# Kernel tuning notes

Hardware: AMD Instinct MI355X
Metric: run time of the kernel (lower is better)

## Reference

```python
import jax, jax.numpy as jnp
import numpy as np

N_NODES = 50000
N_EDGES = 1600000
IN_FEATS = 128
ENC_H = 20
DEC_H = 64


def setup_inputs() -> dict:
    key = jax.random.key(0)
    ks = jax.random.split(key, 14)
    inp = {}
    inp["x"] = jax.random.normal(ks[0], (N_NODES, IN_FEATS), dtype=jnp.float32)
    inp["edge_index"] = jax.random.randint(ks[1], (2, N_EDGES), 0, N_NODES, dtype=jnp.int64)
    inp["node_id"] = 0
    inp["noise_normal"] = jax.random.normal(ks[2], (N_EDGES, ENC_H), dtype=jnp.float32)
    inp["noise_u"] = jax.random.uniform(ks[3], (N_EDGES, 1), dtype=jnp.float32)
    # parameters (glorot-ish init)
    def lin(k, fan_in, fan_out):
        s = 1.0 / np.sqrt(fan_in)
        return jax.random.uniform(k, (fan_in, fan_out), jnp.float32, -s, s)
    inp["W_gc"] = lin(ks[4], IN_FEATS, ENC_H)
    inp["b_gc"] = jnp.zeros((ENC_H,), jnp.float32)
    inp["W_mu"] = lin(ks[5], 3 * ENC_H, ENC_H)
    inp["b_mu"] = jnp.zeros((ENC_H,), jnp.float32)
    inp["W_var"] = lin(ks[6], 3 * ENC_H, ENC_H)
    inp["b_var"] = jnp.zeros((ENC_H,), jnp.float32)
    inp["W_d1"] = lin(ks[7], ENC_H, DEC_H)
    inp["b_d1"] = jnp.zeros((DEC_H,), jnp.float32)
    inp["W_d2"] = lin(ks[8], DEC_H, 1)
    inp["b_d2"] = jnp.zeros((1,), jnp.float32)
    return inp


def _gcn_conv(x, edge_index, W, b):
    """PyG-style GCNConv: add self-loops, symmetric D^-1/2 (A+I) D^-1/2 norm."""
    n = x.shape[0]
    sl = jnp.arange(n, dtype=edge_index.dtype)
    row = jnp.concatenate([edge_index[0], sl])  # source
    col = jnp.concatenate([edge_index[1], sl])  # target
    xw = x @ W  # [N, H]
    deg = jax.ops.segment_sum(jnp.ones_like(col, dtype=xw.dtype), col, num_segments=n)
    dinv = jnp.where(deg > 0, jax.lax.rsqrt(deg), 0.0)
    norm = dinv[row] * dinv[col]  # [E+N]
    out = jax.ops.segment_sum(xw[row] * norm[:, None], col, num_segments=n)
    return out + b


def reference(x, edge_index, node_id, noise_normal, noise_u,
              W_gc, b_gc, W_mu, b_mu, W_var, b_var, W_d1, b_d1, W_d2, b_d2):
    # GCN encoder
    x1 = jax.nn.relu(_gcn_conv(x, edge_index, W_gc, b_gc))  # [N, H]
    # per-edge concat: [src_embed | dst_embed | node_id_embed]
    rows, cols = edge_index[0], edge_index[1]
    node_embed = jnp.broadcast_to(x1[node_id][None, :], (rows.shape[0], x1.shape[1]))
    x2 = jnp.concatenate([x1[rows], x1[cols], node_embed], axis=1)  # [E, 3H]
    # variational heads + reparameterization
    mu = x2 @ W_mu + b_mu
    sigma = jnp.exp(x2 @ W_var + b_var)
    z = mu + sigma * noise_normal  # [E, H]
    # decoder MLP
    h = jax.nn.relu(z @ W_d1 + b_d1)
    sampling_weights = jax.nn.relu(h @ W_d2 + b_d2)  # [E, 1]
    # gumbel-sigmoid sample (training=True, bias=0.0 -> bias'=1e-4, temperature=1.0)
    bias = 0.0001
    eps = (bias - (1.0 - bias)) * noise_u + (1.0 - bias)
    gate = jnp.log(eps) - jnp.log(1.0 - eps) + sampling_weights
    return jax.nn.sigmoid(gate)
```

## Files before the change

### kernel.cpp

```cpp
#include <hip/hip_runtime.h>

#define NFEAT 128
#define H 20
#define DH 64
#define SCAN_T 1024
#define BE 64
#define NB 128
#define HW 12800

typedef __attribute__((ext_vector_type(8))) short short8;
typedef __attribute__((ext_vector_type(4))) float f32x4;

__device__ __forceinline__ unsigned short f2bf(float f) {
    union { float f; unsigned u; } v; v.f = f;
    unsigned r = v.u + 0x7fff + ((v.u >> 16) & 1);
    return (unsigned short)(r >> 16);
}
__device__ __forceinline__ unsigned pk2(unsigned short a, unsigned short b) {
    return (unsigned)a | ((unsigned)b << 16);
}

template <int CTRL>
__device__ __forceinline__ float dpp_add(float x) {
    int y = __builtin_amdgcn_update_dpp(0, __float_as_int(x), CTRL, 0xF, 0xF, true);
    return x + __int_as_float(y);
}
__device__ __forceinline__ float sum16(float x) {
    x = dpp_add<0xB1>(x);
    x = dpp_add<0x4E>(x);
    x = dpp_add<0x124>(x);
    x = dpp_add<0x128>(x);
    return x;
}

__global__ __launch_bounds__(256) void k_prep(const float* __restrict__ Wmu, const float* __restrict__ Wvar,
                                              const float* __restrict__ Wd1,
                                              const float* __restrict__ bmu, const float* __restrict__ bvar,
                                              unsigned short* __restrict__ Bh, unsigned short* __restrict__ Bd1,
                                              float* __restrict__ bcat, int* __restrict__ deg, int N) {
    int t = blockIdx.x * blockDim.x + threadIdx.x;
    if (t < N) deg[t] = 0;
    if (t < 512) {
        int f = t >> 6, l = t & 63;
        int tile = f >> 1, s = f & 1;
        int col = (tile & 1) * 16 + (l & 15);
        const float* W = (tile < 2) ? Wmu : Wvar;
#pragma unroll
        for (int j = 0; j < 8; j++) {
            int k = s * 32 + (l >> 4) * 8 + j;
            float v = (k < 3 * H && col < H) ? W[k * H + col] : 0.f;
            Bh[(size_t)f * 512 + l * 8 + j] = f2bf(v);
        }
    } else if (t < 768) {
        int f = (t - 512) >> 6, l = t & 63;
        int n = f * 16 + (l & 15);
#pragma unroll
        for (int j = 0; j < 8; j++) {
            int k = (l >> 4) * 8 + j;
            float v = (k < H) ? Wd1[k * DH + n] : 0.f;
            Bd1[(size_t)f * 512 + l * 8 + j] = f2bf(v);
        }
    } else if (t < 808) {
        int c = t - 768;
        bcat[c] = (c < H) ? bmu[c] : bvar[c - H];
    }
}


__global__ __launch_bounds__(512) void k_hist(const int* __restrict__ cols,
                                              unsigned* __restrict__ hist, int E, int N) {
    __shared__ unsigned h[HW];
    int wstride = (N + 3) >> 2;
    for (int i = threadIdx.x; i < wstride; i += 512) h[i] = 0;
    __syncthreads();
    int chunk = (E + NB - 1) / NB;
    int beg = blockIdx.x * chunk, end = min(beg + chunk, E);
    for (int i = beg + threadIdx.x; i < end; i += 512) {
        int c = __builtin_nontemporal_load(cols + i);
        atomicAdd(&h[c >> 2], 1u << ((c & 3) * 8));
    }
    __syncthreads();
    unsigned* dst = hist + (size_t)blockIdx.x * wstride;
    for (int i = threadIdx.x; i < wstride; i += 512) dst[i] = h[i];
}

__global__ __launch_bounds__(256) void k_sumbins(const unsigned* __restrict__ hist,
                                                 int* __restrict__ deg, int* __restrict__ chunkSum, int N) {
    __shared__ int sc[256];
    int c = blockIdx.x * 256 + threadIdx.x;
    int wstride = (N + 3) >> 2;
    int sh = (c & 3) * 8;
    int d = 0;
    if (c < N) {
#pragma unroll 4
        for (int b = 0; b < NB; b++) d += (hist[(size_t)b * wstride + (c >> 2)] >> sh) & 0xFF;
        deg[c] = d;
    }
    sc[threadIdx.x] = d;
    __syncthreads();
    for (int off = 128; off > 0; off >>= 1) {
        if (threadIdx.x < off) sc[threadIdx.x] += sc[threadIdx.x + off];
        __syncthreads();
    }
    if (threadIdx.x == 0) chunkSum[blockIdx.x] = sc[0];
}

__global__ __launch_bounds__(256) void k_scansmall(const int* __restrict__ chunkSum,
                                                   int* __restrict__ chunkOff, int nb) {
    __shared__ int sc[256];
    int t = threadIdx.x;
    int v0 = (t < nb) ? chunkSum[t] : 0;
    sc[t] = v0;
    __syncthreads();
    for (int off = 1; off < 256; off <<= 1) {
        int v = (t >= off) ? sc[t - off] : 0;
        __syncthreads();
        sc[t] += v;
        __syncthreads();
    }
    if (t < nb) chunkOff[t] = sc[t] - v0;
}

__global__ __launch_bounds__(256) void k_bases(const unsigned* __restrict__ hist,
                                               const int* __restrict__ chunkOff,
                                               unsigned char* __restrict__ delta,
                                               int* __restrict__ offsets, int N, int E) {
    __shared__ int sc[256];
    int c = blockIdx.x * 256 + threadIdx.x;
    int wstride = (N + 3) >> 2;
    int sh = (c & 3) * 8;
    int d = 0;
    if (c < N) {
#pragma unroll 4
        for (int b = 0; b < NB; b++) d += (hist[(size_t)b * wstride + (c >> 2)] >> sh) & 0xFF;
    }
    sc[threadIdx.x] = d;
    __syncthreads();
    for (int off = 1; off < 256; off <<= 1) {
        int v = (threadIdx.x >= off) ? sc[threadIdx.x - off] : 0;
        __syncthreads();
        sc[threadIdx.x] += v;
        __syncthreads();
    }
    if (c < N) {
        int base = chunkOff[blockIdx.x] + sc[threadIdx.x] - d;
        offsets[c] = base;
        int run = 0;
#pragma unroll 4
        for (int b = 0; b < NB; b++) {
            delta[(size_t)b * N + c] = (unsigned char)run;
            run += (hist[(size_t)b * wstride + (c >> 2)] >> sh) & 0xFF;
        }
    }
    if (blockIdx.x == 0 && threadIdx.x == 0) offsets[N] = E;
}

__global__ __launch_bounds__(512) void k_place(const int* __restrict__ rows, const int* __restrict__ cols,
                                               const int* __restrict__ offsets,
                                               const unsigned char* __restrict__ delta,
                                               unsigned short* __restrict__ srcs, int E, int N) {
    __shared__ unsigned h[HW];
    int wstride = (N + 3) >> 2;
    for (int i = threadIdx.x; i < wstride; i += 512) h[i] = 0;
    __syncthreads();
    int chunk = (E + NB - 1) / NB;
    int beg = blockIdx.x * chunk, end = min(beg + chunk, E);
    const unsigned char* mydelta = delta + (size_t)blockIdx.x * N;
    for (int i = beg + threadIdx.x; i < end; i += 512) {
        int c = __builtin_nontemporal_load(cols + i);
        int r = __builtin_nontemporal_load(rows + i);
        int sh = (c & 3) * 8;
        unsigned old = atomicAdd(&h[c >> 2], 1u << sh);
        int rank = (old >> sh) & 0xFF;
        int pos = offsets[c] + (int)mydelta[c] + rank;
        srcs[pos] = (unsigned short)r;
    }
}

__global__ __launch_bounds__(256) void k_deg(const int* __restrict__ cols, int* __restrict__ deg, int E) {
    int t = blockIdx.x * blockDim.x + threadIdx.x;
    if (t < E) atomicAdd(&deg[cols[t]], 1);
}

__global__ __launch_bounds__(SCAN_T) void k_scan(const int* __restrict__ deg, int* __restrict__ offsets,
                                                 int* __restrict__ cursor, int N) {
    __shared__ int sums[SCAN_T];
    int t = threadIdx.x;
    int chunk = (N + SCAN_T - 1) / SCAN_T;
    int beg = t * chunk;
    int end = min(beg + chunk, N);
    int s = 0;
    for (int i = beg; i < end; i++) s += deg[i];
    sums[t] = s;
    __syncthreads();
    for (int off = 1; off < SCAN_T; off <<= 1) {
        int v = (t >= off) ? sums[t - off] : 0;
        __syncthreads();
        sums[t] += v;
        __syncthreads();
    }
    int run = (t == 0) ? 0 : sums[t - 1];
    for (int i = beg; i < end; i++) {
        offsets[i] = run;
        cursor[i] = run;
        run += deg[i];
    }
    if (t == SCAN_T - 1) offsets[N] = sums[SCAN_T - 1];
}

__global__ __launch_bounds__(256) void k_bucket_csr(const int* __restrict__ rows, const int* __restrict__ cols,
                                                    int* __restrict__ cursor, int* __restrict__ srcs, int E) {
    int e = blockIdx.x * blockDim.x + threadIdx.x;
    if (e >= E) return;
    int pos = atomicAdd(&cursor[cols[e]], 1);
    srcs[pos] = rows[e];
}

__global__ __launch_bounds__(256) void k_xw_xs(const float* __restrict__ x, const float* __restrict__ Wgc,
                                               const int* __restrict__ deg,
                                               float* __restrict__ xs, int N) {
    __shared__ float Ws[NFEAT * H];
    for (int i = threadIdx.x; i < NFEAT * H; i += blockDim.x) Ws[i] = Wgc[i];
    __syncthreads();
    int n = blockIdx.x * blockDim.x + threadIdx.x;
    if (n >= N) return;
    float acc[H];
#pragma unroll
    for (int j = 0; j < H; j++) acc[j] = 0.f;
    const float4* x4 = (const float4*)(x + (size_t)n * NFEAT);
#pragma unroll 4
    for (int k4 = 0; k4 < NFEAT / 4; k4++) {
        float4 xv = x4[k4];
#pragma unroll
        for (int s = 0; s < 4; s++) {
            float xk = (s == 0) ? xv.x : (s == 1) ? xv.y : (s == 2) ? xv.z : xv.w;
            const float4* wrow = (const float4*)(Ws + (k4 * 4 + s) * H);
#pragma unroll
            for (int q = 0; q < 5; q++) {
                float4 w = wrow[q];
                acc[q * 4 + 0] += xk * w.x;
                acc[q * 4 + 1] += xk * w.y;
                acc[q * 4 + 2] += xk * w.z;
                acc[q * 4 + 3] += xk * w.w;
            }
        }
    }
    float di = rsqrtf((float)(deg[n] + 1));
    float4* o = (float4*)(xs + (size_t)n * H);
#pragma unroll
    for (int q = 0; q < 5; q++)
        o[q] = make_float4(acc[q * 4 + 0] * di, acc[q * 4 + 1] * di, acc[q * 4 + 2] * di, acc[q * 4 + 3] * di);
}

template <typename IT>
__device__ __forceinline__ void gather_core16(const float* __restrict__ xs, const IT* __restrict__ idx,
                                              int beg, int end, int n, int sl, int degn,
                                              const float* __restrict__ bgc, unsigned short* __restrict__ x1b) {
    float acc[H];
    if (sl == 0) {
        const float4* self = (const float4*)(xs + (size_t)n * H);
#pragma unroll
        for (int q = 0; q < 5; q++) {
            float4 v = self[q];
            acc[q * 4 + 0] = v.x; acc[q * 4 + 1] = v.y; acc[q * 4 + 2] = v.z; acc[q * 4 + 3] = v.w;
        }
    } else {
#pragma unroll
        for (int j = 0; j < H; j++) acc[j] = 0.f;
    }
#pragma unroll 2
    for (int i = beg + sl; i < end; i += 16) {
        int r = (int)__builtin_nontemporal_load(idx + i);
        const float4* p = (const float4*)(xs + (size_t)r * H);
#pragma unroll
        for (int q = 0; q < 5; q++) {
            float4 v = p[q];
            acc[q * 4 + 0] += v.x; acc[q * 4 + 1] += v.y; acc[q * 4 + 2] += v.z; acc[q * 4 + 3] += v.w;
        }
    }
#pragma unroll
    for (int j = 0; j < H; j++) acc[j] = sum16(acc[j]);
    if (sl == 0) {
        float di = rsqrtf((float)(degn + 1));
        unsigned o[10];
#pragma unroll
        for (int j = 0; j < 10; j++) {
            float v0 = fmaxf(di * acc[2 * j] + bgc[2 * j], 0.f);
            float v1 = fmaxf(di * acc[2 * j + 1] + bgc[2 * j + 1], 0.f);
            o[j] = pk2(f2bf(v0), f2bf(v1));
        }
        unsigned* dst = (unsigned*)(x1b + (size_t)n * H);
        *(uint4*)dst = make_uint4(o[0], o[1], o[2], o[3]);
        *(uint4*)(dst + 4) = make_uint4(o[4], o[5], o[6], o[7]);
        *(uint2*)(dst + 8) = make_uint2(o[8], o[9]);
    }
}

__global__ __launch_bounds__(256) void k_gather_csr16(const float* __restrict__ xs, const unsigned short* __restrict__ srcs,
                                                      const int* __restrict__ offsets, const int* __restrict__ deg,
                                                      const float* __restrict__ bgc,
                                                      unsigned short* __restrict__ x1b, int N) {
    int wave = (blockIdx.x * 256 + threadIdx.x) >> 6;
    int lane = threadIdx.x & 63;
    int n = wave * 4 + (lane >> 4);
    if (n >= N) return;
    gather_core16(xs, srcs, offsets[n], offsets[n + 1], n, lane & 15, deg[n], bgc, x1b);
}

__global__ __launch_bounds__(256) void k_gather_csr(const float* __restrict__ xs, const int* __restrict__ srcs,
                                                    const int* __restrict__ offsets, const int* __restrict__ deg,
                                                    const float* __restrict__ bgc,
                                                    unsigned short* __restrict__ x1b, int N) {
    int wave = (blockIdx.x * 256 + threadIdx.x) >> 6;
    int lane = threadIdx.x & 63;
    int n = wave * 4 + (lane >> 4);
    if (n >= N) return;
    gather_core16(xs, srcs, offsets[n], offsets[n + 1], n, lane & 15, deg[n], bgc, x1b);
}

__global__ __launch_bounds__(256, 8) void k_mlp(
    const unsigned short* __restrict__ x1b, const int* __restrict__ rows, const int* __restrict__ cols,
    const int* __restrict__ node_id, const float* __restrict__ noise_n, const float* __restrict__ noise_u,
    const unsigned short* __restrict__ Bh, const unsigned short* __restrict__ Bd1g,
    const float* __restrict__ bcat, const float* __restrict__ b_d1,
    const float* __restrict__ W_d2, const float* __restrict__ b_d2,
    float* __restrict__ out, int E) {

    __shared__ __align__(16) unsigned short x2s[BE * 72];
    __shared__ __align__(16) unsigned short A2[BE * 44];

    int tid = threadIdx.x;
    int e0 = blockIdx.x * BE;
    int l = tid & 63, w = tid >> 6;
    int m = l & 15, quad = l >> 4;
    int erow0 = w * 16 + quad * 4;

    float nz0[4], nz1[4];
#pragma unroll
    for (int r4 = 0; r4 < 4; r4++) {
        int e = e0 + erow0 + r4;
        int ec = (e < E) ? e : 0;
        nz0[r4] = noise_n[(size_t)ec * H + m];
        nz1[r4] = (m < 4) ? noise_n[(size_t)ec * H + 16 + m] : 0.f;
    }

    {
        int le = tid >> 2, p = tid & 3;
        int e = e0 + le; if (e >= E) e = E - 1;
        int r = rows[e], c = cols[e];
        int nid = node_id[0];
#pragma unroll
        for (int ii = 0; ii < 4; ii++) {
            int i = p + ii * 4;
            unsigned* dst = (unsigned*)((char*)x2s + le * 144 + i * 8);
            if (i < 15) {
                int node = (i < 5) ? r : (i < 10) ? c : nid;
                int cc = (i < 5) ? i : (i < 10) ? i - 5 : i - 10;
                uint2 v = *(const uint2*)((const char*)x1b + (size_t)node * 40 + cc * 8);
                dst[0] = v.x;
                dst[1] = v.y;
            } else {
                dst[0] = 0u; dst[1] = 0u;
            }
        }
    }
    __syncthreads();

    f32x4 accs[4];
    {
        const char* arow = (const char*)x2s + (w * 16 + m) * 144 + quad * 16;
        short8 a0 = *(const short8*)(arow);
        short8 a1 = *(const short8*)(arow + 64);
#pragma unroll
        for (int t4 = 0; t4 < 4; t4++) {
            f32x4 acc = {0.f, 0.f, 0.f, 0.f};
            short8 b0 = *(const short8*)(Bh + (t4 * 2 + 0) * 512 + l * 8);
            short8 b1 = *(const short8*)(Bh + (t4 * 2 + 1) * 512 + l * 8);
            acc = __builtin_amdgcn_mfma_f32_16x16x32_bf16(a0, b0, acc, 0, 0, 0);
            acc = __builtin_amdgcn_mfma_f32_16x16x32_bf16(a1, b1, acc, 0, 0, 0);
            accs[t4] = acc;
        }
    }

    {
        float bm0 = bcat[m];
        float bv0 = bcat[20 + m];
        float bm1 = (m < 4) ? bcat[16 + m] : 0.f;
        float bv1 = (m < 4) ? bcat[36 + m] : 0.f;
#pragma unroll
        for (int r4 = 0; r4 < 4; r4++) {
            float z0 = accs[0][r4] + bm0 + expf(accs[2][r4] + bv0) * nz0[r4];
            *(unsigned short*)((char*)A2 + (erow0 + r4) * 88 + m * 2) = f2bf(z0);
            unsigned short z1v = 0;
            if (m < 4) z1v = f2bf(accs[1][r4] + bm1 + expf(accs[3][r4] + bv1) * nz1[r4]);
            *(unsigned short*)((char*)A2 + (erow0 + r4) * 88 + (16 + m) * 2) = z1v;
        }
    }
    __syncthreads();

    {
        short8 a2 = *(const short8*)((const char*)A2 + (w * 16 + m) * 88 + quad * 16);
        float p0 = 0.f, p1 = 0.f, p2 = 0.f, p3 = 0.f;
#pragma unroll
        for (int t4 = 0; t4 < 4; t4++) {
            f32x4 acc = {0.f, 0.f, 0.f, 0.f};
            short8 bb = *(const short8*)(Bd1g + t4 * 512 + l * 8);
            acc = __builtin_amdgcn_mfma_f32_16x16x32_bf16(a2, bb, acc, 0, 0, 0);
            int col = t4 * 16 + m;
            float bias = b_d1[col], wo = W_d2[col];
            p0 += fmaxf(acc[0] + bias, 0.f) * wo;
            p1 += fmaxf(acc[1] + bias, 0.f) * wo;
            p2 += fmaxf(acc[2] + bias, 0.f) * wo;
            p3 += fmaxf(acc[3] + bias, 0.f) * wo;
        }
        p0 = sum16(p0); p1 = sum16(p1); p2 = sum16(p2); p3 = sum16(p3);
        if (m < 4) {
            float swv = (m == 0) ? p0 : (m == 1) ? p1 : (m == 2) ? p2 : p3;
            int leo = w * 16 + quad * 4 + m;
            int e = e0 + leo;
            if (e < E) {
                float sw = fmaxf(swv + b_d2[0], 0.f);
                float u = noise_u[e];
                float ev = 0.9999f - 0.9998f * u;
                float t = expf(-sw);
                out[e] = ev / (ev + (1.f - ev) * t);
            }
        }
    }
}

extern "C" void kernel_launch(void* const* d_in, const int* in_sizes, int n_in,
                              void* d_out, int out_size, void* d_ws, size_t ws_size,
                              hipStream_t stream) {
    const int N = in_sizes[0] / NFEAT;
    const int E = in_sizes[1] / 2;

    const float* x       = (const float*)d_in[0];
    const int*   ei      = (const int*)d_in[1];
    const int*   rows    = ei;
    const int*   cols    = ei + E;
    const int*   node_id = (const int*)d_in[2];
    const float* noise_n = (const float*)d_in[3];
    const float* noise_u = (const float*)d_in[4];
    const float* Wgc  = (const float*)d_in[5];
    const float* bgc  = (const float*)d_in[6];
    const float* Wmu  = (const float*)d_in[7];
    const float* bmu  = (const float*)d_in[8];
    const float* Wvar = (const float*)d_in[9];
    const float* bvar = (const float*)d_in[10];
    const float* Wd1  = (const float*)d_in[11];
    const float* bd1  = (const float*)d_in[12];
    const float* Wd2  = (const float*)d_in[13];
    const float* bd2  = (const float*)d_in[14];
    float* out = (float*)d_out;

    const int B = 256;
    int gN  = (N + B - 1) / B;
    int gG  = (N + 15) / 16;
    int gE  = (E + B - 1) / B;
    int gM  = (E + BE - 1) / BE;
    int nBins = (N + 255) / 256;

    char* ws = (char*)d_ws;
    size_t o_deg     = 0;
    size_t o_off     = o_deg  + (((size_t)N * 4 + 255) & ~255ULL);
    size_t o_csum    = o_off  + (((size_t)(N + 1) * 4 + 255) & ~255ULL);
    size_t o_coff    = o_csum + 1024;
    size_t o_hist    = o_coff + 1024;
    size_t wstride   = (size_t)((N + 3) >> 2);
    size_t o_delta   = o_hist  + ((NB * wstride * 4 + 255) & ~255ULL);
    size_t o_srcs    = o_delta + (((size_t)NB * N + 255) & ~255ULL);
    size_t o_xs      = o_srcs  + (((size_t)E * 2 + 255) & ~255ULL);
    size_t o_x1b     = o_xs    + (((size_t)N * H * 4 + 255) & ~255ULL);
    size_t o_Bh      = o_x1b   + (((size_t)N * H * 2 + 255) & ~255ULL);
    size_t o_Bd1     = o_Bh    + 8192;
    size_t o_bcat    = o_Bd1   + 4096;
    size_t need      = o_bcat  + 256;

    bool main_path = (ws_size >= need) && (N <= 4 * HW) && (N < 65536) && (nBins <= 256);

    if (main_path) {
        int*   deg     = (int*)(ws + o_deg);
        int*   offsets = (int*)(ws + o_off);
        int*   csum    = (int*)(ws + o_csum);
        int*   coff    = (int*)(ws + o_coff);
        unsigned* hist = (unsigned*)(ws + o_hist);
        unsigned char* delta = (unsigned char*)(ws + o_delta);
        unsigned short* srcs = (unsigned short*)(ws + o_srcs);
        float* xs      = (float*)(ws + o_xs);
        unsigned short* x1b  = (unsigned short*)(ws + o_x1b);
        unsigned short* Bh   = (unsigned short*)(ws + o_Bh);
        unsigned short* Bd1  = (unsigned short*)(ws + o_Bd1);
        float* bcat    = (float*)(ws + o_bcat);

        k_prep<<<gN, B, 0, stream>>>(Wmu, Wvar, Wd1, bmu, bvar, Bh, Bd1, bcat, deg, N);
        k_hist<<<NB, 512, 0, stream>>>(cols, hist, E, N);
        k_sumbins<<<nBins, B, 0, stream>>>(hist, deg, csum, N);
        k_scansmall<<<1, B, 0, stream>>>(csum, coff, nBins);
        k_bases<<<nBins, B, 0, stream>>>(hist, coff, delta, offsets, N, E);
        k_xw_xs<<<gN, B, 0, stream>>>(x, Wgc, deg, xs, N);
        k_place<<<NB, 512, 0, stream>>>(rows, cols, offsets, delta, srcs, E, N);
        k_gather_csr16<<<gG, B, 0, stream>>>(xs, srcs, offsets, deg, bgc, x1b, N);
        k_mlp<<<gM, B, 0, stream>>>(x1b, rows, cols, node_id, noise_n, noise_u,
                                    Bh, Bd1, bcat, bd1, Wd2, bd2, out, E);
    } else {
        int*   deg     = (int*)ws;
        int*   offsets = (int*)(ws + 200000);
        int*   cursor  = (int*)(ws + 400016);
        int*   srcs    = (int*)(ws + 600016);
        float* xs      = (float*)(ws + 7000016);
        unsigned short* x1b = (unsigned short*)(ws + 11000016);
        unsigned short* Bh  = (unsigned short*)(ws + 13000016);
        unsigned short* Bd1 = (unsigned short*)(ws + 13008208);
        float* bcat    = (float*)(ws + 13012304);

        k_prep<<<gN, B, 0, stream>>>(Wmu, Wvar, Wd1, bmu, bvar, Bh, Bd1, bcat, deg, N);
        k_deg<<<gE, B, 0, stream>>>(cols, deg, E);
        k_scan<<<1, SCAN_T, 0, stream>>>(deg, offsets, cursor, N);
        k_bucket_csr<<<gE, B, 0, stream>>>(rows, cols, cursor, srcs, E);
        k_xw_xs<<<gN, B, 0, stream>>>(x, Wgc, deg, xs, N);
        k_gather_csr<<<gG, B, 0, stream>>>(xs, srcs, offsets, deg, bgc, x1b, N);
        k_mlp<<<gM, B, 0, stream>>>(x1b, rows, cols, node_id, noise_n, noise_u,
                                    Bh, Bd1, bcat, bd1, Wd2, bd2, out, E);
    }
}
```

Measured before the change: 448.2 us.

## Fold node_id embedding into head bias, fuse degree sums into histogram pass

The node_id third of the concatenated edge feature is the same for every edge, so its product with W_mu/W_var is computed once by the thread handling node_id in the gather kernel and folded into a per-call bias. The per-edge MLP then drops that gather and the K dimension shrinks to 40. The k_sumbins pass is removed: chunk sums are accumulated atomically in k_hist, and k_bases keeps per-bin counts in registers to write deg and the delta table without re-reading hist. NB grows to 192 and expf becomes __expf, which trades a little accuracy and adds register pressure in k_bases.

```diff
diff --git a/kernel.cpp b/kernel.cpp
--- a/kernel.cpp
+++ b/kernel.cpp
@@ -5,7 +5,7 @@
 #define DH 64
 #define SCAN_T 1024
 #define BE 64
-#define NB 128
+#define NB 192
 #define HW 12800
 
 typedef __attribute__((ext_vector_type(8))) short short8;
@@ -35,11 +35,11 @@
 
 __global__ __launch_bounds__(256) void k_prep(const float* __restrict__ Wmu, const float* __restrict__ Wvar,
                                               const float* __restrict__ Wd1,
-                                              const float* __restrict__ bmu, const float* __restrict__ bvar,
                                               unsigned short* __restrict__ Bh, unsigned short* __restrict__ Bd1,
-                                              float* __restrict__ bcat, int* __restrict__ deg, int N) {
+                                              int* __restrict__ deg, int* __restrict__ csum, int N) {
     int t = blockIdx.x * blockDim.x + threadIdx.x;
     if (t < N) deg[t] = 0;
+    if (t < 256) csum[t] = 0;
     if (t < 512) {
         int f = t >> 6, l = t & 63;
         int tile = f >> 1, s = f & 1;
@@ -48,7 +48,7 @@
 #pragma unroll
         for (int j = 0; j < 8; j++) {
             int k = s * 32 + (l >> 4) * 8 + j;
-            float v = (k < 3 * H && col < H) ? W[k * H + col] : 0.f;
+            float v = (k < 2 * H && col < H) ? W[k * H + col] : 0.f;
             Bh[(size_t)f * 512 + l * 8 + j] = f2bf(v);
         }
     } else if (t < 768) {
@@ -60,18 +60,18 @@
             float v = (k < H) ? Wd1[k * DH + n] : 0.f;
             Bd1[(size_t)f * 512 + l * 8 + j] = f2bf(v);
         }
-    } else if (t < 808) {
-        int c = t - 768;
-        bcat[c] = (c < H) ? bmu[c] : bvar[c - H];
-    }
-}
-
+    }
+}
 
 __global__ __launch_bounds__(512) void k_hist(const int* __restrict__ cols,
-                                              unsigned* __restrict__ hist, int E, int N) {
+                                              unsigned* __restrict__ hist, int* __restrict__ csum,
+                                              int E, int N) {
     __shared__ unsigned h[HW];
+    __shared__ int cs[256];
     int wstride = (N + 3) >> 2;
+    int nchunks = (N + 255) >> 8;
     for (int i = threadIdx.x; i < wstride; i += 512) h[i] = 0;
+    if (threadIdx.x < 256) cs[threadIdx.x] = 0;
     __syncthreads();
     int chunk = (E + NB - 1) / NB;
     int beg = blockIdx.x * chunk, end = min(beg + chunk, E);
@@ -81,28 +81,17 @@
     }
     __syncthreads();
     unsigned* dst = hist + (size_t)blockIdx.x * wstride;
-    for (int i = threadIdx.x; i < wstride; i += 512) dst[i] = h[i];
-}
-
-__global__ __launch_bounds__(256) void k_sumbins(const unsigned* __restrict__ hist,
-                                                 int* __restrict__ deg, int* __restrict__ chunkSum, int N) {
-    __shared__ int sc[256];
-    int c = blockIdx.x * 256 + threadIdx.x;
-    int wstride = (N + 3) >> 2;
-    int sh = (c & 3) * 8;
-    int d = 0;
-    if (c < N) {
-#pragma unroll 4
-        for (int b = 0; b < NB; b++) d += (hist[(size_t)b * wstride + (c >> 2)] >> sh) & 0xFF;
-        deg[c] = d;
-    }
-    sc[threadIdx.x] = d;
-    __syncthreads();
-    for (int off = 128; off > 0; off >>= 1) {
-        if (threadIdx.x < off) sc[threadIdx.x] += sc[threadIdx.x + off];
-        __syncthreads();
-    }
-    if (threadIdx.x == 0) chunkSum[blockIdx.x] = sc[0];
+    for (int i = threadIdx.x; i < wstride; i += 512) {
+        unsigned w = h[i];
+        dst[i] = w;
+        if (w) {
+            int s = (w & 0xFF) + ((w >> 8) & 0xFF) + ((w >> 16) & 0xFF) + (w >> 24);
+            atomicAdd(&cs[i >> 6], s);
+        }
+    }
+    __syncthreads();
+    for (int j = threadIdx.x; j < nchunks; j += 512)
+        if (cs[j]) atomicAdd(&csum[j], cs[j]);
 }
 
 __global__ __launch_bounds__(256) void k_scansmall(const int* __restrict__ chunkSum,
@@ -124,16 +113,25 @@
 __global__ __launch_bounds__(256) void k_bases(const unsigned* __restrict__ hist,
                                                const int* __restrict__ chunkOff,
                                                unsigned char* __restrict__ delta,
-                                               int* __restrict__ offsets, int N, int E) {
+                                               int* __restrict__ offsets, int* __restrict__ deg,
+                                               int N, int E) {
     __shared__ int sc[256];
     int c = blockIdx.x * 256 + threadIdx.x;
     int wstride = (N + 3) >> 2;
     int sh = (c & 3) * 8;
+    bool valid = c < N;
+    int cw = valid ? (c >> 2) : 0;
+    unsigned cnt[NB / 4];
     int d = 0;
-    if (c < N) {
-#pragma unroll 4
-        for (int b = 0; b < NB; b++) d += (hist[(size_t)b * wstride + (c >> 2)] >> sh) & 0xFF;
-    }
+#pragma unroll
+    for (int b = 0; b < NB; b++) {
+        unsigned w = hist[(size_t)b * wstride + cw];
+        unsigned byte = (w >> sh) & 0xFF;
+        if ((b & 3) == 0) cnt[b >> 2] = byte;
+        else cnt[b >> 2] |= byte << ((b & 3) * 8);
+        d += (int)byte;
+    }
+    if (!valid) d = 0;
     sc[threadIdx.x] = d;
     __syncthreads();
     for (int off = 1; off < 256; off <<= 1) {
@@ -142,14 +140,15 @@
         sc[threadIdx.x] += v;
         __syncthreads();
     }
-    if (c < N) {
+    if (valid) {
         int base = chunkOff[blockIdx.x] + sc[threadIdx.x] - d;
         offsets[c] = base;
+        deg[c] = d;
         int run = 0;
-#pragma unroll 4
+#pragma unroll
         for (int b = 0; b < NB; b++) {
             delta[(size_t)b * N + c] = (unsigned char)run;
-            run += (hist[(size_t)b * wstride + (c >> 2)] >> sh) & 0xFF;
+            run += (int)((cnt[b >> 2] >> ((b & 3) * 8)) & 0xFF);
         }
     }
     if (blockIdx.x == 0 && threadIdx.x == 0) offsets[N] = E;
@@ -255,7 +254,10 @@
 template <typename IT>
 __device__ __forceinline__ void gather_core16(const float* __restrict__ xs, const IT* __restrict__ idx,
                                               int beg, int end, int n, int sl, int degn,
-                                              const float* __restrict__ bgc, unsigned short* __restrict__ x1b) {
+                                              const float* __restrict__ bgc, unsigned short* __restrict__ x1b,
+                                              int nid, const float* __restrict__ Wmu, const float* __restrict__ Wvar,
+                                              const float* __restrict__ bmu, const float* __restrict__ bvar,
+                                              float* __restrict__ bcat2) {
     float acc[H];
     if (sl == 0) {
         const float4* self = (const float4*)(xs + (size_t)n * H);
@@ -280,49 +282,73 @@
     }
 #pragma unroll
     for (int j = 0; j < H; j++) acc[j] = sum16(acc[j]);
+    float di = rsqrtf((float)(degn + 1));
+    float x1f[H];
+#pragma unroll
+    for (int j = 0; j < H; j++) x1f[j] = fmaxf(di * acc[j] + bgc[j], 0.f);
     if (sl == 0) {
-        float di = rsqrtf((float)(degn + 1));
         unsigned o[10];
 #pragma unroll
-        for (int j = 0; j < 10; j++) {
-            float v0 = fmaxf(di * acc[2 * j] + bgc[2 * j], 0.f);
-            float v1 = fmaxf(di * acc[2 * j + 1] + bgc[2 * j + 1], 0.f);
-            o[j] = pk2(f2bf(v0), f2bf(v1));
-        }
+        for (int j = 0; j < 10; j++) o[j] = pk2(f2bf(x1f[2 * j]), f2bf(x1f[2 * j + 1]));
         unsigned* dst = (unsigned*)(x1b + (size_t)n * H);
         *(uint4*)dst = make_uint4(o[0], o[1], o[2], o[3]);
         *(uint4*)(dst + 4) = make_uint4(o[4], o[5], o[6], o[7]);
         *(uint2*)(dst + 8) = make_uint2(o[8], o[9]);
     }
+    if (n == nid) {
+#pragma unroll
+        for (int base = 0; base < 48; base += 16) {
+            int jj = base + sl;
+            if (jj < 40) {
+                bool ismu = jj < 20;
+                int col = ismu ? jj : jj - 20;
+                const float* W = ismu ? Wmu : Wvar;
+                float s = ismu ? bmu[col] : bvar[col];
+#pragma unroll
+                for (int k = 0; k < H; k++) s += x1f[k] * W[(2 * H + k) * H + col];
+                bcat2[jj] = s;
+            }
+        }
+    }
 }
 
 __global__ __launch_bounds__(256) void k_gather_csr16(const float* __restrict__ xs, const unsigned short* __restrict__ srcs,
                                                       const int* __restrict__ offsets, const int* __restrict__ deg,
                                                       const float* __restrict__ bgc,
-                                                      unsigned short* __restrict__ x1b, int N) {
+                                                      unsigned short* __restrict__ x1b,
+                                                      const int* __restrict__ node_id,
+                                                      const float* __restrict__ Wmu, const float* __restrict__ Wvar,
+                                                      const float* __restrict__ bmu, const float* __restrict__ bvar,
+                                                      float* __restrict__ bcat2, int N) {
     int wave = (blockIdx.x * 256 + threadIdx.x) >> 6;
     int lane = threadIdx.x & 63;
     int n = wave * 4 + (lane >> 4);
     if (n >= N) return;
-    gather_core16(xs, srcs, offsets[n], offsets[n + 1], n, lane & 15, deg[n], bgc, x1b);
+    gather_core16(xs, srcs, offsets[n], offsets[n + 1], n, lane & 15, deg[n], bgc, x1b,
+                  node_id[0], Wmu, Wvar, bmu, bvar, bcat2);
 }
 
 __global__ __launch_bounds__(256) void k_gather_csr(const float* __restrict__ xs, const int* __restrict__ srcs,
                                                     const int* __restrict__ offsets, const int* __restrict__ deg,
                                                     const float* __restrict__ bgc,
-                                                    unsigned short* __restrict__ x1b, int N) {
+                                                    unsigned short* __restrict__ x1b,
+                                                    const int* __restrict__ node_id,
+                                                    const float* __restrict__ Wmu, const float* __restrict__ Wvar,
+                                                    const float* __restrict__ bmu, const float* __restrict__ bvar,
+                                                    float* __restrict__ bcat2, int N) {
     int wave = (blockIdx.x * 256 + threadIdx.x) >> 6;
     int lane = threadIdx.x & 63;
     int n = wave * 4 + (lane >> 4);
     if (n >= N) return;
-    gather_core16(xs, srcs, offsets[n], offsets[n + 1], n, lane & 15, deg[n], bgc, x1b);
+    gather_core16(xs, srcs, offsets[n], offsets[n + 1], n, lane & 15, deg[n], bgc, x1b,
+                  node_id[0], Wmu, Wvar, bmu, bvar, bcat2);
 }
 
 __global__ __launch_bounds__(256, 8) void k_mlp(
     const unsigned short* __restrict__ x1b, const int* __restrict__ rows, const int* __restrict__ cols,
-    const int* __restrict__ node_id, const float* __restrict__ noise_n, const float* __restrict__ noise_u,
+    const float* __restrict__ noise_n, const float* __restrict__ noise_u,
     const unsigned short* __restrict__ Bh, const unsigned short* __restrict__ Bd1g,
-    const float* __restrict__ bcat, const float* __restrict__ b_d1,
+    const float* __restrict__ bcat2, const float* __restrict__ b_d1,
     const float* __restrict__ W_d2, const float* __restrict__ b_d2,
     float* __restrict__ out, int E) {
 
@@ -348,14 +374,13 @@
         int le = tid >> 2, p = tid & 3;
         int e = e0 + le; if (e >= E) e = E - 1;
         int r = rows[e], c = cols[e];
-        int nid = node_id[0];
 #pragma unroll
         for (int ii = 0; ii < 4; ii++) {
             int i = p + ii * 4;
             unsigned* dst = (unsigned*)((char*)x2s + le * 144 + i * 8);
-            if (i < 15) {
-                int node = (i < 5) ? r : (i < 10) ? c : nid;
-                int cc = (i < 5) ? i : (i < 10) ? i - 5 : i - 10;
+            if (i < 10) {
+                int node = (i < 5) ? r : c;
+                int cc = (i < 5) ? i : i - 5;
                 uint2 v = *(const uint2*)((const char*)x1b + (size_t)node * 40 + cc * 8);
                 dst[0] = v.x;
                 dst[1] = v.y;
@@ -383,16 +408,16 @@
     }
 
     {
-        float bm0 = bcat[m];
-        float bv0 = bcat[20 + m];
-        float bm1 = (m < 4) ? bcat[16 + m] : 0.f;
-        float bv1 = (m < 4) ? bcat[36 + m] : 0.f;
+        float bm0 = bcat2[m];
+        float bv0 = bcat2[20 + m];
+        float bm1 = (m < 4) ? bcat2[16 + m] : 0.f;
+        float bv1 = (m < 4) ? bcat2[36 + m] : 0.f;
 #pragma unroll
         for (int r4 = 0; r4 < 4; r4++) {
-            float z0 = accs[0][r4] + bm0 + expf(accs[2][r4] + bv0) * nz0[r4];
+            float z0 = accs[0][r4] + bm0 + __expf(accs[2][r4] + bv0) * nz0[r4];
             *(unsigned short*)((char*)A2 + (erow0 + r4) * 88 + m * 2) = f2bf(z0);
             unsigned short z1v = 0;
-            if (m < 4) z1v = f2bf(accs[1][r4] + bm1 + expf(accs[3][r4] + bv1) * nz1[r4]);
+            if (m < 4) z1v = f2bf(accs[1][r4] + bm1 + __expf(accs[3][r4] + bv1) * nz1[r4]);
             *(unsigned short*)((char*)A2 + (erow0 + r4) * 88 + (16 + m) * 2) = z1v;
         }
     }
@@ -422,7 +447,7 @@
                 float sw = fmaxf(swv + b_d2[0], 0.f);
                 float u = noise_u[e];
                 float ev = 0.9999f - 0.9998f * u;
-                float t = expf(-sw);
+                float t = __expf(-sw);
                 out[e] = ev / (ev + (1.f - ev) * t);
             }
         }
@@ -474,8 +499,8 @@
     size_t o_x1b     = o_xs    + (((size_t)N * H * 4 + 255) & ~255ULL);
     size_t o_Bh      = o_x1b   + (((size_t)N * H * 2 + 255) & ~255ULL);
     size_t o_Bd1     = o_Bh    + 8192;
-    size_t o_bcat    = o_Bd1   + 4096;
-    size_t need      = o_bcat  + 256;
+    size_t o_bcat2   = o_Bd1   + 4096;
+    size_t need      = o_bcat2 + 256;
 
     bool main_path = (ws_size >= need) && (N <= 4 * HW) && (N < 65536) && (nBins <= 256);
 
@@ -491,18 +516,18 @@
         unsigned short* x1b  = (unsigned short*)(ws + o_x1b);
         unsigned short* Bh   = (unsigned short*)(ws + o_Bh);
         unsigned short* Bd1  = (unsigned short*)(ws + o_Bd1);
-        float* bcat    = (float*)(ws + o_bcat);
-
-        k_prep<<<gN, B, 0, stream>>>(Wmu, Wvar, Wd1, bmu, bvar, Bh, Bd1, bcat, deg, N);
-        k_hist<<<NB, 512, 0, stream>>>(cols, hist, E, N);
-        k_sumbins<<<nBins, B, 0, stream>>>(hist, deg, csum, N);
+        float* bcat2   = (float*)(ws + o_bcat2);
+
+        k_prep<<<gN, B, 0, stream>>>(Wmu, Wvar, Wd1, Bh, Bd1, deg, csum, N);
+        k_hist<<<NB, 512, 0, stream>>>(cols, hist, csum, E, N);
         k_scansmall<<<1, B, 0, stream>>>(csum, coff, nBins);
-        k_bases<<<nBins, B, 0, stream>>>(hist, coff, delta, offsets, N, E);
+        k_bases<<<nBins, B, 0, stream>>>(hist, coff, delta, offsets, deg, N, E);
         k_xw_xs<<<gN, B, 0, stream>>>(x, Wgc, deg, xs, N);
         k_place<<<NB, 512, 0, stream>>>(rows, cols, offsets, delta, srcs, E, N);
-        k_gather_csr16<<<gG, B, 0, stream>>>(xs, srcs, offsets, deg, bgc, x1b, N);
-        k_mlp<<<gM, B, 0, stream>>>(x1b, rows, cols, node_id, noise_n, noise_u,
-                                    Bh, Bd1, bcat, bd1, Wd2, bd2, out, E);
+        k_gather_csr16<<<gG, B, 0, stream>>>(xs, srcs, offsets, deg, bgc, x1b,
+                                             node_id, Wmu, Wvar, bmu, bvar, bcat2, N);
+        k_mlp<<<gM, B, 0, stream>>>(x1b, rows, cols, noise_n, noise_u,
+                                    Bh, Bd1, bcat2, bd1, Wd2, bd2, out, E);
     } else {
         int*   deg     = (int*)ws;
         int*   offsets = (int*)(ws + 200000);
@@ -512,15 +537,16 @@
         unsigned short* x1b = (unsigned short*)(ws + 11000016);
         unsigned short* Bh  = (unsigned short*)(ws + 13000016);
         unsigned short* Bd1 = (unsigned short*)(ws + 13008208);
-        float* bcat    = (float*)(ws + 13012304);
-
-        k_prep<<<gN, B, 0, stream>>>(Wmu, Wvar, Wd1, bmu, bvar, Bh, Bd1, bcat, deg, N);
+        float* bcat2   = (float*)(ws + 13012304);
+
+        k_prep<<<gN, B, 0, stream>>>(Wmu, Wvar, Wd1, Bh, Bd1, deg, cursor, N);
         k_deg<<<gE, B, 0, stream>>>(cols, deg, E);
         k_scan<<<1, SCAN_T, 0, stream>>>(deg, offsets, cursor, N);
         k_bucket_csr<<<gE, B, 0, stream>>>(rows, cols, cursor, srcs, E);
         k_xw_xs<<<gN, B, 0, stream>>>(x, Wgc, deg, xs, N);
-        k_gather_csr<<<gG, B, 0, stream>>>(xs, srcs, offsets, deg, bgc, x1b, N);
-        k_mlp<<<gM, B, 0, stream>>>(x1b, rows, cols, node_id, noise_n, noise_u,
-                                    Bh, Bd1, bcat, bd1, Wd2, bd2, out, E);
-    }
-}
+        k_gather_csr<<<gG, B, 0, stream>>>(xs, srcs, offsets, deg, bgc, x1b,
+                                           node_id, Wmu, Wvar, bmu, bvar, bcat2, N);
+        k_mlp<<<gM, B, 0, stream>>>(x1b, rows, cols, noise_n, noise_u,
+                                    Bh, Bd1, bcat2, bd1, Wd2, bd2, out, E);
+    }
+}
```

Result: faster. 430.4 us (-4.0%).
